# Optimization experiments

Hardware: AMD Instinct MI355X
Metric: run time of the kernel (lower is better)

## Reference

```python
import jax, jax.numpy as jnp
import numpy as np

# comb = (l1=3, l2=3, lo=2, k=2): contract the last k spatial indices of T1
# with the first k spatial indices of T2. PATH_=4 is index 'a', batch 'b',
# channel 'c'. Normalizer = 1/sqrt(3**k) = 1/3.
PATH_ = 4
BATCH_ = 131072
CHANNEL_ = 6
EXPR = 'abcdef,bcefg->abcdg'
NORMALIZER = 1.0 / np.sqrt(3.0 ** 2)


def setup_inputs() -> dict:
    key = jax.random.key(0)
    k1, k2 = jax.random.split(key)
    T1 = jax.random.normal(k1, (PATH_, BATCH_, CHANNEL_, 3, 3, 3), dtype=jnp.float32)
    T2 = jax.random.normal(k2, (BATCH_, CHANNEL_, 3, 3, 3), dtype=jnp.float32)
    return {"T1": T1, "T2": T2}


def reference(T1, T2):
    # single fused einsum: contract spatial indices e,f; broadcast path 'a'
    # over T2; batch 'b' and channel 'c' are elementwise-shared.
    out = jnp.einsum(EXPR, T1, T2)
    return out * jnp.asarray(NORMALIZER, dtype=out.dtype)
```

## Files before the change

kernel.cpp:

```cpp
#include <hip/hip_runtime.h>


#define A_        4
#define BC_       786432
#define TILE_     64
#define NTHREADS  256

#define SEG_BYTES    6912
#define CHUNK_BYTES  1024
#define FULL_CHUNKS  6
#define TAIL_LANES   48
#define NCHUNK       35

#define T1_A_BYTES     84934656u
#define OUT_A_STRIDE4  1769472
#define OUT_TILE4      144

__device__ __forceinline__ void load_lds16(const void* g, void* l) {
    __builtin_amdgcn_global_load_lds(
        (const __attribute__((address_space(1))) void*)g,
        (__attribute__((address_space(3))) void*)l,
        16, 0, 0);
}

__global__ __launch_bounds__(NTHREADS, 4)
void prod_einsum_kernel(const float* __restrict__ T1,
                        const float* __restrict__ T2,
                        float* __restrict__ Out) {
    __shared__ float smem[8640];
    float4* smem4 = (float4*)smem;
    float4* Outv  = (float4*)Out;

    const int tid  = threadIdx.x;
    const int lane = tid & 63;
    const int wave = tid >> 6;
    const int blk  = blockIdx.x;

    {
        const char* t1b  = (const char*)T1 + (size_t)blk * SEG_BYTES;
        const char* t2b  = (const char*)T2 + (size_t)blk * SEG_BYTES;
        char*       lds0 = (char*)smem;
        for (int c = wave; c < NCHUNK; c += 4) {
            const int s = c / 7;
            const int k = c - s * 7;
            const char* gseg = (s < 4) ? (t1b + (size_t)s * T1_A_BYTES) : t2b;
            const char* gsrc = gseg + k * CHUNK_BYTES + lane * 16;
            char*       ldst = lds0 + s * SEG_BYTES + k * CHUNK_BYTES;
            if (k < FULL_CHUNKS) {
                load_lds16(gsrc, ldst);
            } else if (lane < TAIL_LANES) {
                load_lds16(gsrc, ldst);
            }
        }
    }
    __syncthreads();

    const int a = tid >> 6;
    const int l = tid & 63;
    const float* t1 = smem + (a * TILE_ + l) * 27;
    const float* t2 = smem + 6912 + l * 27;

    float r1[27], r2[27];
    #pragma unroll
    for (int i = 0; i < 27; ++i) r1[i] = t1[i];
    #pragma unroll
    for (int i = 0; i < 27; ++i) r2[i] = t2[i];

    float acc[9];
    #pragma unroll
    for (int d = 0; d < 3; ++d) {
        #pragma unroll
        for (int g = 0; g < 3; ++g) {
            float s = 0.0f;
            #pragma unroll
            for (int e = 0; e < 3; ++e) {
                #pragma unroll
                for (int f = 0; f < 3; ++f) {
                    s += r1[d * 9 + e * 3 + f] * r2[e * 9 + f * 3 + g];
                }
            }
            acc[d * 3 + g] = s * (1.0f / 3.0f);
        }
    }

    __syncthreads();

    #pragma unroll
    for (int i = 0; i < 9; ++i) {
        smem[(a * TILE_ + l) * 9 + i] = acc[i];
    }
    __syncthreads();

    for (int j = tid; j < 4 * OUT_TILE4; j += NTHREADS) {
        int a2 = j / OUT_TILE4;
        int r  = j - a2 * OUT_TILE4;
        Outv[a2 * OUT_A_STRIDE4 + blk * OUT_TILE4 + r] = smem4[j];
    }
}

extern "C" void kernel_launch(void* const* d_in, const int* in_sizes, int n_in,
                              void* d_out, int out_size, void* d_ws, size_t ws_size,
                              hipStream_t stream) {
    const float* T1 = (const float*)d_in[0];
    const float* T2 = (const float*)d_in[1];
    float* Out = (float*)d_out;
    prod_einsum_kernel<<<BC_ / TILE_, NTHREADS, 0, stream>>>(T1, T2, Out);
}
```

Baseline: 518.1 us.

## Make kernel persistent with double-buffered async LDS staging across tiles

Replaces one-tile-per-block launch with 512 persistent blocks each processing 24 tiles. The next tile's T1/T2 data is prefetched into a second LDS buffer via global_load_lds, with hand-tuned vmcnt waits, while the current tile is computed and stored. The aim is to hide global load latency and cut block launch overhead. In exchange it uses roughly twice the LDS, lowers occupancy to two blocks per CU, and depends on fragile manual waitcnt counts that must match the number of issued loads and stores.

```diff
diff --git a/kernel.cpp b/kernel.cpp
--- a/kernel.cpp
+++ b/kernel.cpp
@@ -5,6 +5,8 @@
 #define BC_       786432
 #define TILE_     64
 #define NTHREADS  256
+#define NBLOCKS   512
+#define TPB       24
 
 #define SEG_BYTES    6912
 #define CHUNK_BYTES  1024
@@ -16,85 +18,120 @@
 #define OUT_A_STRIDE4  1769472
 #define OUT_TILE4      144
 
+#define BUF_FLOATS   8640
+#define OUT_OFF      (2 * BUF_FLOATS)
+#define SMEM_FLOATS  (2 * BUF_FLOATS + 2304)
+
+#define WAITV(n) asm volatile("s_waitcnt vmcnt(" #n ")" ::: "memory")
+#define CFENCE() asm volatile("" ::: "memory")
+
 __device__ __forceinline__ void load_lds16(const void* g, void* l) {
     __builtin_amdgcn_global_load_lds(
         (const __attribute__((address_space(1))) void*)g,
-        (__attribute__((address_space(3))) void*)l,
-        16, 0, 0);
+        (__attribute__((address_space(3))) void*)l, 16, 0, 0);
 }
 
-__global__ __launch_bounds__(NTHREADS, 4)
+__device__ __forceinline__ void stage_tile(const char* t1base, const char* t2base,
+                                           int tile, float* buf,
+                                           int wave, int lane) {
+    const char* t1b = t1base + (size_t)tile * SEG_BYTES;
+    const char* t2b = t2base + (size_t)tile * SEG_BYTES;
+    char* lds0 = (char*)buf;
+    const int c0 = wave * 9;
+    const int c1 = (c0 + 9 < NCHUNK) ? (c0 + 9) : NCHUNK;
+    for (int c = c0; c < c1; ++c) {
+        const int s = c / 7;
+        const int k = c - s * 7;
+        const char* gseg = (s < 4) ? (t1b + (size_t)s * T1_A_BYTES) : t2b;
+        const char* gsrc = gseg + k * CHUNK_BYTES + lane * 16;
+        char*       ldst = lds0 + s * SEG_BYTES + k * CHUNK_BYTES;
+        if (k < FULL_CHUNKS) {
+            load_lds16(gsrc, ldst);
+        } else if (lane < TAIL_LANES) {
+            load_lds16(gsrc, ldst);
+        }
+    }
+}
+
+__global__ __launch_bounds__(NTHREADS, 2)
 void prod_einsum_kernel(const float* __restrict__ T1,
                         const float* __restrict__ T2,
                         float* __restrict__ Out) {
-    __shared__ float smem[8640];
-    float4* smem4 = (float4*)smem;
-    float4* Outv  = (float4*)Out;
+    __shared__ float smem[SMEM_FLOATS];
+    float4* Outv = (float4*)Out;
 
     const int tid  = threadIdx.x;
     const int lane = tid & 63;
     const int wave = tid >> 6;
-    const int blk  = blockIdx.x;
+    const int a    = wave;
+    const int l    = lane;
+    const int t0   = blockIdx.x * TPB;
 
-    {
-        const char* t1b  = (const char*)T1 + (size_t)blk * SEG_BYTES;
-        const char* t2b  = (const char*)T2 + (size_t)blk * SEG_BYTES;
-        char*       lds0 = (char*)smem;
-        for (int c = wave; c < NCHUNK; c += 4) {
-            const int s = c / 7;
-            const int k = c - s * 7;
-            const char* gseg = (s < 4) ? (t1b + (size_t)s * T1_A_BYTES) : t2b;
-            const char* gsrc = gseg + k * CHUNK_BYTES + lane * 16;
-            char*       ldst = lds0 + s * SEG_BYTES + k * CHUNK_BYTES;
-            if (k < FULL_CHUNKS) {
-                load_lds16(gsrc, ldst);
-            } else if (lane < TAIL_LANES) {
-                load_lds16(gsrc, ldst);
+    const char* t1base = (const char*)T1;
+    const char* t2base = (const char*)T2;
+
+    stage_tile(t1base, t2base, t0, smem, wave, lane);
+
+    for (int i = 0; i < TPB; ++i) {
+        float* bufc = smem + (i & 1) * BUF_FLOATS;
+
+        if (i + 1 < TPB)
+            stage_tile(t1base, t2base, t0 + i + 1,
+                       smem + ((i + 1) & 1) * BUF_FLOATS, wave, lane);
+
+        if (i == 0) {
+            if (i + 1 < TPB) { if (wave == 3) WAITV(8); else WAITV(9); }
+            else             { WAITV(0); }
+        } else if (i + 1 < TPB) {
+            if (wave == 0)      WAITV(12);
+            else if (wave == 3) WAITV(10);
+            else                WAITV(11);
+        } else {
+            if (wave == 0) WAITV(3); else WAITV(2);
+        }
+        __builtin_amdgcn_s_barrier();
+        CFENCE();
+
+        const float* t1 = bufc + (a * TILE_ + l) * 27;
+        const float* t2 = bufc + 4 * TILE_ * 27 + l * 27;
+        float r1[27], r2[27];
+        #pragma unroll
+        for (int q = 0; q < 27; ++q) r1[q] = t1[q];
+        #pragma unroll
+        for (int q = 0; q < 27; ++q) r2[q] = t2[q];
+
+        float acc[9];
+        #pragma unroll
+        for (int d = 0; d < 3; ++d) {
+            #pragma unroll
+            for (int g = 0; g < 3; ++g) {
+                float s = 0.0f;
+                #pragma unroll
+                for (int e = 0; e < 3; ++e) {
+                    #pragma unroll
+                    for (int f = 0; f < 3; ++f) {
+                        s += r1[d * 9 + e * 3 + f] * r2[e * 9 + f * 3 + g];
+                    }
+                }
+                acc[d * 3 + g] = s * (1.0f / 3.0f);
             }
         }
-    }
-    __syncthreads();
 
-    const int a = tid >> 6;
-    const int l = tid & 63;
-    const float* t1 = smem + (a * TILE_ + l) * 27;
-    const float* t2 = smem + 6912 + l * 27;
+        #pragma unroll
+        for (int q = 0; q < 9; ++q) {
+            smem[OUT_OFF + (a * TILE_ + l) * 9 + q] = acc[q];
+        }
+        asm volatile("s_waitcnt lgkmcnt(0)" ::: "memory");
+        __builtin_amdgcn_s_barrier();
+        CFENCE();
 
-    float r1[27], r2[27];
-    #pragma unroll
-    for (int i = 0; i < 27; ++i) r1[i] = t1[i];
-    #pragma unroll
-    for (int i = 0; i < 27; ++i) r2[i] = t2[i];
-
-    float acc[9];
-    #pragma unroll
-    for (int d = 0; d < 3; ++d) {
-        #pragma unroll
-        for (int g = 0; g < 3; ++g) {
-            float s = 0.0f;
-            #pragma unroll
-            for (int e = 0; e < 3; ++e) {
-                #pragma unroll
-                for (int f = 0; f < 3; ++f) {
-                    s += r1[d * 9 + e * 3 + f] * r2[e * 9 + f * 3 + g];
-                }
-            }
-            acc[d * 3 + g] = s * (1.0f / 3.0f);
+        const float4* outs = (const float4*)(smem + OUT_OFF);
+        const int tgt = t0 + i;
+        for (int j = tid; j < 4 * OUT_TILE4; j += NTHREADS) {
+            const int a2 = j / OUT_TILE4;
+            const int r  = j - a2 * OUT_TILE4;
+            Outv[a2 * OUT_A_STRIDE4 + (size_t)tgt * OUT_TILE4 + r] = outs[j];
         }
-    }
-
-    __syncthreads();
-
-    #pragma unroll
-    for (int i = 0; i < 9; ++i) {
-        smem[(a * TILE_ + l) * 9 + i] = acc[i];
-    }
-    __syncthreads();
-
-    for (int j = tid; j < 4 * OUT_TILE4; j += NTHREADS) {
-        int a2 = j / OUT_TILE4;
-        int r  = j - a2 * OUT_TILE4;
-        Outv[a2 * OUT_A_STRIDE4 + blk * OUT_TILE4 + r] = smem4[j];
     }
 }
 
@@ -104,5 +141,5 @@
     const float* T1 = (const float*)d_in[0];
     const float* T2 = (const float*)d_in[1];
     float* Out = (float*)d_out;
-    prod_einsum_kernel<<<BC_ / TILE_, NTHREADS, 0, stream>>>(T1, T2, Out);
+    prod_einsum_kernel<<<NBLOCKS, NTHREADS, 0, stream>>>(T1, T2, Out);
 }
```

Result: slower. 530.5 us (+2.4%).
